# Performance work log

Measured on AMD Instinct MI355X. Metric: run time of the kernel, lower is better.

## Reference

```python
import jax, jax.numpy as jnp
import numpy as np

BASE_LR = 0.1
LN_EPS = 1e-5
D_IN = 1024
D_OUT = 1024
BATCH = 16384


def setup_inputs() -> dict:
    key = jax.random.key(0)
    ks = jax.random.split(key, 5)
    x = jax.random.normal(ks[0], (BATCH, D_IN), dtype=jnp.float32)
    plasticity = jax.random.uniform(ks[1], (BATCH,), dtype=jnp.float32)
    alpha = jax.random.uniform(ks[2], (1,), dtype=jnp.float32)
    # Parameters / buffers (orthogonal / kaiming init approximated with scaled normals)
    W_slow = jax.random.normal(ks[3], (D_OUT, D_IN), dtype=jnp.float32) * (1.4 / np.sqrt(D_IN))
    bound = 1.0 / np.sqrt(D_IN)  # kaiming_uniform with a=sqrt(5) on [d_out, d_in]
    W_fast = jax.random.uniform(ks[4], (D_OUT, D_IN), dtype=jnp.float32, minval=-bound, maxval=bound)
    gamma = jnp.ones((D_OUT,), dtype=jnp.float32)
    beta = jnp.zeros((D_OUT,), dtype=jnp.float32)
    return {"x": x, "plasticity": plasticity, "alpha": alpha,
            "W_slow": W_slow, "W_fast": W_fast, "gamma": gamma, "beta": beta}


def reference(x, plasticity, alpha, W_slow, W_fast, gamma, beta):
    # Dual linear reads: [B, d_in] @ [d_in, d_out]
    slow = x @ W_slow.T           # [B, d_out]
    fast = x @ W_fast.T           # [B, d_out]

    # Hebbian fast-weight update (training branch, no-grad in original)
    batch = x.shape[0]
    hebb = (fast.T @ x) / batch                         # [d_out, d_in]
    forget = jnp.mean(fast ** 2, axis=0)[:, None] * W_fast  # [d_out, d_in]
    eff_lr = jnp.mean(plasticity) * BASE_LR             # scalar, kept on-device
    W_fast_new = W_fast + jnp.tanh(hebb - forget) * eff_lr

    # Combine + LayerNorm over last dim
    combined = slow + fast * alpha                      # alpha broadcast scalar
    mu = jnp.mean(combined, axis=-1, keepdims=True)
    var = jnp.mean((combined - mu) ** 2, axis=-1, keepdims=True)
    out = (combined - mu) * jax.lax.rsqrt(var + LN_EPS) * gamma + beta
    return (out, slow, W_fast_new)
```

## Files before the change

kernel.cpp:

```cpp
#include <hip/hip_runtime.h>
#include <cstdint>
#include <cstddef>

#define B_SZ 16384
#define DIN  1024
#define DOUT 1024
#define SPLITK 16

typedef short bf16x8 __attribute__((ext_vector_type(8)));
typedef float f32x4  __attribute__((ext_vector_type(4)));

static __device__ __forceinline__ short f2bf(float f) {
    union { float f; unsigned u; } v; v.f = f;
    unsigned r = v.u + 0x7fffu + ((v.u >> 16) & 1u);
    return (short)(r >> 16);
}
static __device__ __forceinline__ float bf2f(short s) {
    union { unsigned u; float f; } v; v.u = ((unsigned)(unsigned short)s) << 16;
    return v.f;
}
static __device__ __forceinline__ void gload_lds16(const short* g, short* l) {
    __builtin_amdgcn_global_load_lds(
        (const __attribute__((address_space(1))) void*)g,
        (__attribute__((address_space(3))) void*)l, 16, 0, 0);
}

__global__ __launch_bounds__(256) void convert_w2(const float* __restrict__ wsl,
                                                  const float* __restrict__ wfa,
                                                  short* __restrict__ out) {
    const int half = DOUT * DIN / 4;
    int i = blockIdx.x * 256 + threadIdx.x;
    const float* src = (i < half) ? wsl : wfa;
    int j = (i < half) ? i : i - half;
    float4 v = ((const float4*)src)[j];
    short4 o;
    o.x = f2bf(v.x); o.y = f2bf(v.y); o.z = f2bf(v.z); o.w = f2bf(v.w);
    ((short4*)out)[i] = o;
}

__global__ __launch_bounds__(256) void x_convert(const float* __restrict__ x,
                                                 short* __restrict__ xb,
                                                 short* __restrict__ xT) {
    __shared__ short t[64 * 72];
    const int b0 = blockIdx.x * 64;
    const int d0 = blockIdx.y * 64;
    const int tid = threadIdx.x;
    const int r = tid >> 2;
    const int c = (tid & 3) * 16;
    short loc[16];
    #pragma unroll
    for (int i = 0; i < 4; ++i) {
        float4 v = *(const float4*)&x[(size_t)(b0 + r) * DIN + d0 + c + i * 4];
        loc[i * 4 + 0] = f2bf(v.x); loc[i * 4 + 1] = f2bf(v.y);
        loc[i * 4 + 2] = f2bf(v.z); loc[i * 4 + 3] = f2bf(v.w);
    }
    *(bf16x8*)&xb[(size_t)(b0 + r) * DIN + d0 + c]     = *(bf16x8*)&loc[0];
    *(bf16x8*)&xb[(size_t)(b0 + r) * DIN + d0 + c + 8] = *(bf16x8*)&loc[8];
    #pragma unroll
    for (int i = 0; i < 16; ++i) t[(c + i) * 72 + r] = loc[i];
    __syncthreads();
    const int d = tid >> 2, bs = (tid & 3) * 16;
    *(bf16x8*)&xT[(size_t)(d0 + d) * B_SZ + b0 + bs]     = *(bf16x8*)&t[d * 72 + bs];
    *(bf16x8*)&xT[(size_t)(d0 + d) * B_SZ + b0 + bs + 8] = *(bf16x8*)&t[d * 72 + bs + 8];
}

__global__ __launch_bounds__(256) void fast_trans(const float* __restrict__ fast,
                                                  short* __restrict__ fastT) {
    __shared__ short t[64 * 72];
    const int b0 = blockIdx.x * 64;
    const int d0 = blockIdx.y * 64;
    const int tid = threadIdx.x;
    const int r = tid >> 2;
    const int c = (tid & 3) * 16;
    short loc[16];
    #pragma unroll
    for (int i = 0; i < 4; ++i) {
        float4 v = *(const float4*)&fast[(size_t)(b0 + r) * DOUT + d0 + c + i * 4];
        loc[i * 4 + 0] = f2bf(v.x); loc[i * 4 + 1] = f2bf(v.y);
        loc[i * 4 + 2] = f2bf(v.z); loc[i * 4 + 3] = f2bf(v.w);
    }
    #pragma unroll
    for (int i = 0; i < 16; ++i) t[(c + i) * 72 + r] = loc[i];
    __syncthreads();
    const int d = tid >> 2, bs = (tid & 3) * 16;
    *(bf16x8*)&fastT[(size_t)(d0 + d) * B_SZ + b0 + bs]     = *(bf16x8*)&t[d * 72 + bs];
    *(bf16x8*)&fastT[(size_t)(d0 + d) * B_SZ + b0 + bs + 8] = *(bf16x8*)&t[d * 72 + bs + 8];
}

__global__ __launch_bounds__(256) void init_kernel(const float* __restrict__ plast,
                                                   float* __restrict__ eff_lr,
                                                   float* __restrict__ csq) {
    int tid = threadIdx.x;
    for (int i = tid; i < DOUT; i += 256) csq[i] = 0.f;
    float s = 0.f;
    for (int i = tid; i < B_SZ; i += 256) s += plast[i];
    __shared__ float red[256];
    red[tid] = s; __syncthreads();
    for (int off = 128; off > 0; off >>= 1) {
        if (tid < off) red[tid] += red[tid + off];
        __syncthreads();
    }
    if (tid == 0) eff_lr[0] = (red[0] / (float)B_SZ) * 0.1f;
}

#define PRIO1 __builtin_amdgcn_s_setprio(1)
#define PRIO0 __builtin_amdgcn_s_setprio(0)
#define BARX  asm volatile("s_barrier" ::: "memory")
#define LGKM0 asm volatile("s_waitcnt lgkmcnt(0)" ::: "memory")
#define VMC4  asm volatile("s_waitcnt vmcnt(4)" ::: "memory")
#define VMC0  asm volatile("s_waitcnt vmcnt(0)" ::: "memory")

#define STG(RO, SRC, LD, KT, H) do { \
    const short* _s = (SRC) + (size_t)((H) * 128 + srow) * (LD) + (KT) * 64 + scol; \
    gload_lds16(_s, &L[(RO) + ((H) * 128 + wrow8) * 64]); \
    gload_lds16(_s + (size_t)64 * (LD), &L[(RO) + ((H) * 128 + 64 + wrow8) * 64]); \
} while (0)

#define RDA(RO, MH) do { \
    const int _rb = (RO) + (wm * 128 + (MH) * 64 + l16) * 64; \
    _Pragma("unroll") for (int mf = 0; mf < 4; ++mf) { \
        a_[mf][0] = *(const bf16x8*)&L[_rb + mf * 1024 + c0]; \
        a_[mf][1] = *(const bf16x8*)&L[_rb + mf * 1024 + (c0 ^ 32)]; \
    } \
} while (0)

#define RDB(RO, NH) do { \
    const int _rb = (RO) + (wn * 64 + (NH) * 32 + l16) * 64; \
    _Pragma("unroll") for (int nf = 0; nf < 2; ++nf) { \
        b_[NH][nf][0] = *(const bf16x8*)&L[_rb + nf * 1024 + c0]; \
        b_[NH][nf][1] = *(const bf16x8*)&L[_rb + nf * 1024 + (c0 ^ 32)]; \
    } \
} while (0)

#define MM(MH, NH) do { \
    _Pragma("unroll") for (int mf = 0; mf < 4; ++mf) \
    _Pragma("unroll") for (int nf = 0; nf < 2; ++nf) { \
        acc[(MH)*4+mf][(NH)*2+nf] = __builtin_amdgcn_mfma_f32_16x16x32_bf16(a_[mf][0], b_[NH][nf][0], acc[(MH)*4+mf][(NH)*2+nf], 0, 0, 0); \
        acc[(MH)*4+mf][(NH)*2+nf] = __builtin_amdgcn_mfma_f32_16x16x32_bf16(a_[mf][1], b_[NH][nf][1], acc[(MH)*4+mf][(NH)*2+nf], 0, 0, 0); \
    } \
} while (0)

template<int EPI>
static __device__ __forceinline__ void gemm256_core(
    const short* __restrict__ Asrc, int lda,
    const short* __restrict__ Bsrc, int ldb,
    float* __restrict__ dstf,
    short* __restrict__ dsth,
    int m0, int cb)
{
    __shared__ short L[65536];
    const int A0o = 0, A1o = 16384, B0o = 32768, B1o = 49152;
    const int tid  = threadIdx.x;
    const int lane = tid & 63;
    const int w    = tid >> 6;
    const int wm   = w >> 2;
    const int wn   = w & 3;
    const int quad = lane >> 4;
    const int l16  = lane & 15;
    const int c0   = ((quad ^ (l16 & 7)) << 3);
    const int wrow8 = w * 8;
    const int srow  = tid >> 3;
    const int scol  = (((lane & 7) ^ (lane >> 3)) << 3);

    f32x4 acc[8][4] = {};
    bf16x8 a_[4][2];
    bf16x8 b_[2][2][2];

    STG(B0o, Bsrc, ldb, 0, 0); STG(B0o, Bsrc, ldb, 0, 1);
    STG(A0o, Asrc, lda, 0, 0); STG(A0o, Asrc, lda, 0, 1);
    STG(B1o, Bsrc, ldb, 1, 0); STG(B1o, Bsrc, ldb, 1, 1);
    VMC4; BARX;

    for (int it = 0; it < 7; ++it) {
        const int t = 2 * it;
        RDA(A0o, 0); RDB(B0o, 0); STG(A1o, Asrc, lda, t + 1, 0);
        BARX; LGKM0; PRIO1; MM(0, 0); PRIO0; BARX;
        RDB(B0o, 1); STG(A1o, Asrc, lda, t + 1, 1);
        BARX; LGKM0; PRIO1; MM(0, 1); PRIO0; BARX;
        RDA(A0o, 1); STG(B0o, Bsrc, ldb, t + 2, 0);
        BARX; LGKM0; PRIO1; MM(1, 1); PRIO0; BARX;
        STG(B0o, Bsrc, ldb, t + 2, 1);
        BARX; PRIO1; MM(1, 0); PRIO0; VMC4; BARX;
        RDA(A1o, 0); RDB(B1o, 0); STG(A0o, Asrc, lda, t + 2, 0);
        BARX; LGKM0; PRIO1; MM(0, 0); PRIO0; BARX;
        RDB(B1o, 1); STG(A0o, Asrc, lda, t + 2, 1);
        BARX; LGKM0; PRIO1; MM(0, 1); PRIO0; BARX;
        RDA(A1o, 1); STG(B1o, Bsrc, ldb, t + 3, 0);
        BARX; LGKM0; PRIO1; MM(1, 1); PRIO0; BARX;
        STG(B1o, Bsrc, ldb, t + 3, 1);
        BARX; PRIO1; MM(1, 0); PRIO0; VMC4; BARX;
    }
    RDA(A0o, 0); RDB(B0o, 0); STG(A1o, Asrc, lda, 15, 0);
    BARX; LGKM0; PRIO1; MM(0, 0); PRIO0; BARX;
    RDB(B0o, 1); STG(A1o, Asrc, lda, 15, 1);
    BARX; LGKM0; PRIO1; MM(0, 1); PRIO0; BARX;
    RDA(A0o, 1);
    BARX; LGKM0; PRIO1; MM(1, 1); PRIO0; BARX;
    BARX; PRIO1; MM(1, 0); PRIO0; VMC0; BARX;
    RDA(A1o, 0); RDB(B1o, 0);
    BARX; LGKM0; PRIO1; MM(0, 0); PRIO0; BARX;
    RDB(B1o, 1);
    BARX; LGKM0; PRIO1; MM(0, 1); PRIO0; BARX;
    RDA(A1o, 1);
    BARX; LGKM0; PRIO1; MM(1, 1); PRIO0; BARX;
    PRIO1; MM(1, 0); PRIO0;

    if (EPI == 0) {
        #pragma unroll
        for (int mf = 0; mf < 8; ++mf) {
            const int r0 = m0 + wm * 128 + mf * 16 + quad * 4;
            #pragma unroll
            for (int nf = 0; nf < 4; ++nf) {
                const int cc = cb + wn * 64 + nf * 16 + l16;
                #pragma unroll
                for (int r = 0; r < 4; ++r)
                    dstf[(size_t)(r0 + r) * 1024 + cc] = acc[mf][nf][r];
            }
        }
    } else {
        #pragma unroll
        for (int mf = 0; mf < 8; ++mf) {
            const int r0 = m0 + wm * 128 + mf * 16 + quad * 4;
            #pragma unroll
            for (int nf = 0; nf < 4; ++nf) {
                const int cc = cb + wn * 64 + nf * 16 + l16;
                #pragma unroll
                for (int r = 0; r < 4; ++r)
                    dsth[(size_t)(r0 + r) * DIN + cc] = f2bf(acc[mf][nf][r]);
            }
        }
    }
}

__global__ __launch_bounds__(512) void dual_gemm8(
    const short* __restrict__ Xb, const short* __restrict__ Wc,
    float* __restrict__ slow_out, float* __restrict__ fast_out)
{
    const int bid = blockIdx.x;
    const int id  = (bid & 7) * 64 + (bid >> 3);
    const int bm  = id & 63, bn = id >> 6;
    const int m0  = bm * 256, n0 = bn * 256;
    float* dst = (n0 < 1024) ? slow_out : fast_out;
    gemm256_core<0>(&Xb[(size_t)m0 * DIN], DIN, &Wc[(size_t)n0 * DIN], DIN,
                    dst, nullptr, m0, n0 & 1023);
}

__global__ __launch_bounds__(512) void hebb_gemm8(
    const short* __restrict__ fastT, const short* __restrict__ xT,
    short* __restrict__ hebb_part)
{
    const int m0 = blockIdx.x * 256;
    const int n0 = blockIdx.y * 256;
    const size_t kb = (size_t)blockIdx.z * (B_SZ / SPLITK);
    gemm256_core<1>(&fastT[(size_t)m0 * B_SZ + kb], B_SZ,
                    &xT[(size_t)n0 * B_SZ + kb], B_SZ,
                    nullptr, hebb_part + (size_t)blockIdx.z * DOUT * DIN, m0, n0);
}

__global__ __launch_bounds__(256) void colsumsq_kernel(const short* __restrict__ fastT,
                                                       float* __restrict__ sums) {
    const int m = blockIdx.x;
    const int tid = threadIdx.x;
    const short* row = &fastT[(size_t)m * B_SZ];
    float s = 0.f;
    for (int i = tid * 8; i < B_SZ; i += 256 * 8) {
        bf16x8 v = *(const bf16x8*)&row[i];
        #pragma unroll
        for (int j = 0; j < 8; ++j) { float f = bf2f(v[j]); s += f * f; }
    }
    __shared__ float red[256];
    red[tid] = s; __syncthreads();
    for (int off = 128; off > 0; off >>= 1) {
        if (tid < off) red[tid] += red[tid + off];
        __syncthreads();
    }
    if (tid == 0) sums[m] = red[0];
}

__global__ __launch_bounds__(256) void wfast_update(
    const float* __restrict__ Wf, const short* __restrict__ hebb_part,
    const float* __restrict__ colsumsq, const float* __restrict__ eff_lr,
    float* __restrict__ Wf_new)
{
    const int i0 = (blockIdx.x * 256 + threadIdx.x) * 8;
    const int m = i0 >> 10;
    const float lr = eff_lr[0];
    const float fgm = colsumsq[m] * (1.0f / (float)B_SZ);
    float h[8] = {0.f, 0.f, 0.f, 0.f, 0.f, 0.f, 0.f, 0.f};
    #pragma unroll
    for (int z = 0; z < SPLITK; ++z) {
        bf16x8 v = *(const bf16x8*)&hebb_part[(size_t)z * DOUT * DIN + i0];
        #pragma unroll
        for (int j = 0; j < 8; ++j) h[j] += bf2f(v[j]);
    }
    float4 w0 = *(const float4*)&Wf[i0];
    float4 w1 = *(const float4*)&Wf[i0 + 4];
    float w[8] = {w0.x, w0.y, w0.z, w0.w, w1.x, w1.y, w1.z, w1.w};
    float o[8];
    #pragma unroll
    for (int j = 0; j < 8; ++j)
        o[j] = w[j] + tanhf(h[j] * (1.0f / (float)B_SZ) - fgm * w[j]) * lr;
    *(float4*)&Wf_new[i0]     = make_float4(o[0], o[1], o[2], o[3]);
    *(float4*)&Wf_new[i0 + 4] = make_float4(o[4], o[5], o[6], o[7]);
}

__global__ __launch_bounds__(256) void ln_kernel(
    const float* __restrict__ slow, float* __restrict__ io,
    const float* __restrict__ gamma, const float* __restrict__ beta,
    const float* __restrict__ alpha)
{
    const int row = blockIdx.x;
    const int tid = threadIdx.x;
    const float a = alpha[0];
    const size_t base = (size_t)row * DOUT;
    float c[4];
    float s = 0.f, ss = 0.f;
    #pragma unroll
    for (int i = 0; i < 4; ++i) {
        int col = tid + i * 256;
        float v = slow[base + col] + a * io[base + col];
        c[i] = v; s += v; ss += v * v;
    }
    #pragma unroll
    for (int off = 32; off > 0; off >>= 1) {
        s  += __shfl_down(s, off);
        ss += __shfl_down(ss, off);
    }
    __shared__ float rs[4], rss[4];
    int wave = tid >> 6;
    if ((tid & 63) == 0) { rs[wave] = s; rss[wave] = ss; }
    __syncthreads();
    float S  = rs[0] + rs[1] + rs[2] + rs[3];
    float SS = rss[0] + rss[1] + rss[2] + rss[3];
    float mu = S * (1.0f / DOUT);
    float var = SS * (1.0f / DOUT) - mu * mu;
    float inv = rsqrtf(var + 1e-5f);
    #pragma unroll
    for (int i = 0; i < 4; ++i) {
        int col = tid + i * 256;
        io[base + col] = (c[i] - mu) * inv * gamma[col] + beta[col];
    }
}

extern "C" void kernel_launch(void* const* d_in, const int* in_sizes, int n_in,
                              void* d_out, int out_size, void* d_ws, size_t ws_size,
                              hipStream_t stream)
{
    const float* x     = (const float*)d_in[0];
    const float* plast = (const float*)d_in[1];
    const float* alpha = (const float*)d_in[2];
    const float* Wslow = (const float*)d_in[3];
    const float* Wfast = (const float*)d_in[4];
    const float* gamma = (const float*)d_in[5];
    const float* beta  = (const float*)d_in[6];

    float* out   = (float*)d_out;
    float* slow  = out + (size_t)B_SZ * DOUT;
    float* wfnew = slow + (size_t)B_SZ * DOUT;

    char* ws = (char*)d_ws;
    const size_t SZ_XB   = (size_t)B_SZ * DIN * 2;
    const size_t SZ_XT   = (size_t)DIN * B_SZ * 2;
    const size_t SZ_WCAT = (size_t)2048 * DIN * 2;
    const size_t SZ_HEBB = (size_t)SPLITK * DOUT * DIN * 2;
    short* xb    = (short*)ws;
    short* fastT = xb;
    short* xT    = (short*)(ws + SZ_XB);
    short* wcat  = (short*)(ws + SZ_XB + SZ_XT);
    short* hebb  = (short*)(ws + SZ_XB + SZ_XT + SZ_WCAT);
    float* csq   = (float*)(ws + SZ_XB + SZ_XT + SZ_WCAT + SZ_HEBB);
    float* efflr = csq + DOUT;

    x_convert<<<dim3(B_SZ / 64, DIN / 64), 256, 0, stream>>>(x, xb, xT);
    convert_w2<<<(2 * DOUT * DIN / 4) / 256, 256, 0, stream>>>(Wslow, Wfast, wcat);
    init_kernel<<<1, 256, 0, stream>>>(plast, efflr, csq);
    dual_gemm8<<<512, 512, 0, stream>>>(xb, wcat, slow, out);
    fast_trans<<<dim3(B_SZ / 64, DOUT / 64), 256, 0, stream>>>(out, fastT);
    colsumsq_kernel<<<DOUT, 256, 0, stream>>>(fastT, csq);
    hebb_gemm8<<<dim3(DOUT / 256, DIN / 256, SPLITK), 512, 0, stream>>>(fastT, xT, hebb);
    wfast_update<<<(DOUT * DIN) / (256 * 8), 256, 0, stream>>>(Wfast, hebb, csq, efflr, wfnew);
    ln_kernel<<<B_SZ, 256, 0, stream>>>(slow, out, gamma, beta, alpha);
}
```

Before: 397.6 us.

## Emit fast output as bf16, fuse transpose with column sum-of-squares, remap hebb grid

The dual GEMM now writes the fast projection as bf16 into workspace rather than fp32 into the output buffer. The transpose kernel reads those bf16 values and accumulates the per-column sum of squares with atomics, which removes the separate colsumsq pass over fastT. LayerNorm reads the bf16 fast values and runs before the hebb GEMM so the fastb buffer can be reused for hebb partials. Hebb GEMM blocks are swizzled across split-K slices, and the shared LDS array moved out to the kernels. The trade-off is lower precision in the combined LayerNorm input and nondeterministic atomic summation.

```diff
diff --git a/kernel.cpp b/kernel.cpp
--- a/kernel.cpp
+++ b/kernel.cpp
@@ -64,27 +64,31 @@
     *(bf16x8*)&xT[(size_t)(d0 + d) * B_SZ + b0 + bs + 8] = *(bf16x8*)&t[d * 72 + bs + 8];
 }
 
-__global__ __launch_bounds__(256) void fast_trans(const float* __restrict__ fast,
-                                                  short* __restrict__ fastT) {
+__global__ __launch_bounds__(256) void ft_cs(const short* __restrict__ fastb,
+                                             short* __restrict__ fastT,
+                                             float* __restrict__ csq) {
     __shared__ short t[64 * 72];
     const int b0 = blockIdx.x * 64;
     const int d0 = blockIdx.y * 64;
     const int tid = threadIdx.x;
     const int r = tid >> 2;
     const int c = (tid & 3) * 16;
-    short loc[16];
-    #pragma unroll
-    for (int i = 0; i < 4; ++i) {
-        float4 v = *(const float4*)&fast[(size_t)(b0 + r) * DOUT + d0 + c + i * 4];
-        loc[i * 4 + 0] = f2bf(v.x); loc[i * 4 + 1] = f2bf(v.y);
-        loc[i * 4 + 2] = f2bf(v.z); loc[i * 4 + 3] = f2bf(v.w);
-    }
-    #pragma unroll
-    for (int i = 0; i < 16; ++i) t[(c + i) * 72 + r] = loc[i];
+    bf16x8 v0 = *(const bf16x8*)&fastb[(size_t)(b0 + r) * DOUT + d0 + c];
+    bf16x8 v1 = *(const bf16x8*)&fastb[(size_t)(b0 + r) * DOUT + d0 + c + 8];
+    #pragma unroll
+    for (int i = 0; i < 8; ++i) { t[(c + i) * 72 + r] = v0[i]; t[(c + 8 + i) * 72 + r] = v1[i]; }
     __syncthreads();
     const int d = tid >> 2, bs = (tid & 3) * 16;
-    *(bf16x8*)&fastT[(size_t)(d0 + d) * B_SZ + b0 + bs]     = *(bf16x8*)&t[d * 72 + bs];
-    *(bf16x8*)&fastT[(size_t)(d0 + d) * B_SZ + b0 + bs + 8] = *(bf16x8*)&t[d * 72 + bs + 8];
+    bf16x8 o0 = *(const bf16x8*)&t[d * 72 + bs];
+    bf16x8 o1 = *(const bf16x8*)&t[d * 72 + bs + 8];
+    *(bf16x8*)&fastT[(size_t)(d0 + d) * B_SZ + b0 + bs]     = o0;
+    *(bf16x8*)&fastT[(size_t)(d0 + d) * B_SZ + b0 + bs + 8] = o1;
+    float p = 0.f;
+    #pragma unroll
+    for (int i = 0; i < 8; ++i) { float a = bf2f(o0[i]), b = bf2f(o1[i]); p += a * a + b * b; }
+    p += __shfl_down(p, 2);
+    p += __shfl_down(p, 1);
+    if ((tid & 3) == 0) atomicAdd(&csq[d0 + d], p);
 }
 
 __global__ __launch_bounds__(256) void init_kernel(const float* __restrict__ plast,
@@ -142,13 +146,13 @@
 
 template<int EPI>
 static __device__ __forceinline__ void gemm256_core(
+    short* L,
     const short* __restrict__ Asrc, int lda,
     const short* __restrict__ Bsrc, int ldb,
     float* __restrict__ dstf,
     short* __restrict__ dsth,
     int m0, int cb)
 {
-    __shared__ short L[65536];
     const int A0o = 0, A1o = 16384, B0o = 32768, B1o = 49152;
     const int tid  = threadIdx.x;
     const int lane = tid & 63;
@@ -234,47 +238,36 @@
 
 __global__ __launch_bounds__(512) void dual_gemm8(
     const short* __restrict__ Xb, const short* __restrict__ Wc,
-    float* __restrict__ slow_out, float* __restrict__ fast_out)
-{
+    float* __restrict__ slow_out, short* __restrict__ fastb)
+{
+    __shared__ short L[65536];
     const int bid = blockIdx.x;
     const int id  = (bid & 7) * 64 + (bid >> 3);
     const int bm  = id & 63, bn = id >> 6;
     const int m0  = bm * 256, n0 = bn * 256;
-    float* dst = (n0 < 1024) ? slow_out : fast_out;
-    gemm256_core<0>(&Xb[(size_t)m0 * DIN], DIN, &Wc[(size_t)n0 * DIN], DIN,
-                    dst, nullptr, m0, n0 & 1023);
+    if (n0 < 1024)
+        gemm256_core<0>(L, &Xb[(size_t)m0 * DIN], DIN, &Wc[(size_t)n0 * DIN], DIN,
+                        slow_out, nullptr, m0, n0);
+    else
+        gemm256_core<1>(L, &Xb[(size_t)m0 * DIN], DIN, &Wc[(size_t)n0 * DIN], DIN,
+                        nullptr, fastb, m0, n0 - 1024);
 }
 
 __global__ __launch_bounds__(512) void hebb_gemm8(
     const short* __restrict__ fastT, const short* __restrict__ xT,
     short* __restrict__ hebb_part)
 {
-    const int m0 = blockIdx.x * 256;
-    const int n0 = blockIdx.y * 256;
-    const size_t kb = (size_t)blockIdx.z * (B_SZ / SPLITK);
-    gemm256_core<1>(&fastT[(size_t)m0 * B_SZ + kb], B_SZ,
+    __shared__ short L[65536];
+    const int bid = blockIdx.x;
+    const int id  = (bid & 7) * 32 + (bid >> 3);
+    const int z   = id >> 4;
+    const int mn  = id & 15;
+    const int m0  = (mn >> 2) * 256;
+    const int n0  = (mn & 3) * 256;
+    const size_t kb = (size_t)z * (B_SZ / SPLITK);
+    gemm256_core<1>(L, &fastT[(size_t)m0 * B_SZ + kb], B_SZ,
                     &xT[(size_t)n0 * B_SZ + kb], B_SZ,
-                    nullptr, hebb_part + (size_t)blockIdx.z * DOUT * DIN, m0, n0);
-}
-
-__global__ __launch_bounds__(256) void colsumsq_kernel(const short* __restrict__ fastT,
-                                                       float* __restrict__ sums) {
-    const int m = blockIdx.x;
-    const int tid = threadIdx.x;
-    const short* row = &fastT[(size_t)m * B_SZ];
-    float s = 0.f;
-    for (int i = tid * 8; i < B_SZ; i += 256 * 8) {
-        bf16x8 v = *(const bf16x8*)&row[i];
-        #pragma unroll
-        for (int j = 0; j < 8; ++j) { float f = bf2f(v[j]); s += f * f; }
-    }
-    __shared__ float red[256];
-    red[tid] = s; __syncthreads();
-    for (int off = 128; off > 0; off >>= 1) {
-        if (tid < off) red[tid] += red[tid + off];
-        __syncthreads();
-    }
-    if (tid == 0) sums[m] = red[0];
+                    nullptr, hebb_part + (size_t)z * DOUT * DIN, m0, n0);
 }
 
 __global__ __launch_bounds__(256) void wfast_update(
@@ -304,8 +297,9 @@
     *(float4*)&Wf_new[i0 + 4] = make_float4(o[4], o[5], o[6], o[7]);
 }
 
-__global__ __launch_bounds__(256) void ln_kernel(
-    const float* __restrict__ slow, float* __restrict__ io,
+__global__ __launch_bounds__(256) void ln2_kernel(
+    const float* __restrict__ slow, const short* __restrict__ fastb,
+    float* __restrict__ out,
     const float* __restrict__ gamma, const float* __restrict__ beta,
     const float* __restrict__ alpha)
 {
@@ -318,7 +312,7 @@
     #pragma unroll
     for (int i = 0; i < 4; ++i) {
         int col = tid + i * 256;
-        float v = slow[base + col] + a * io[base + col];
+        float v = slow[base + col] + a * bf2f(fastb[base + col]);
         c[i] = v; s += v; ss += v * v;
     }
     #pragma unroll
@@ -338,7 +332,7 @@
     #pragma unroll
     for (int i = 0; i < 4; ++i) {
         int col = tid + i * 256;
-        io[base + col] = (c[i] - mu) * inv * gamma[col] + beta[col];
+        out[base + col] = (c[i] - mu) * inv * gamma[col] + beta[col];
     }
 }
 
@@ -367,17 +361,17 @@
     short* fastT = xb;
     short* xT    = (short*)(ws + SZ_XB);
     short* wcat  = (short*)(ws + SZ_XB + SZ_XT);
-    short* hebb  = (short*)(ws + SZ_XB + SZ_XT + SZ_WCAT);
+    short* fastb = (short*)(ws + SZ_XB + SZ_XT + SZ_WCAT);
+    short* hebb  = fastb;
     float* csq   = (float*)(ws + SZ_XB + SZ_XT + SZ_WCAT + SZ_HEBB);
     float* efflr = csq + DOUT;
 
     x_convert<<<dim3(B_SZ / 64, DIN / 64), 256, 0, stream>>>(x, xb, xT);
     convert_w2<<<(2 * DOUT * DIN / 4) / 256, 256, 0, stream>>>(Wslow, Wfast, wcat);
     init_kernel<<<1, 256, 0, stream>>>(plast, efflr, csq);
-    dual_gemm8<<<512, 512, 0, stream>>>(xb, wcat, slow, out);
-    fast_trans<<<dim3(B_SZ / 64, DOUT / 64), 256, 0, stream>>>(out, fastT);
-    colsumsq_kernel<<<DOUT, 256, 0, stream>>>(fastT, csq);
-    hebb_gemm8<<<dim3(DOUT / 256, DIN / 256, SPLITK), 512, 0, stream>>>(fastT, xT, hebb);
+    dual_gemm8<<<512, 512, 0, stream>>>(xb, wcat, slow, fastb);
+    ft_cs<<<dim3(B_SZ / 64, DOUT / 64), 256, 0, stream>>>(fastb, fastT, csq);
+    ln2_kernel<<<B_SZ, 256, 0, stream>>>(slow, fastb, out, gamma, beta, alpha);
+    hebb_gemm8<<<256, 512, 0, stream>>>(fastT, xT, hebb);
     wfast_update<<<(DOUT * DIN) / (256 * 8), 256, 0, stream>>>(Wfast, hebb, csq, efflr, wfnew);
-    ln_kernel<<<B_SZ, 256, 0, stream>>>(slow, out, gamma, beta, alpha);
-}
+}
```

Result: no change. 396.7 us (-0.2%).
